# Performance work log

Hardware: AMD Instinct MI355X
Metric: run time of the kernel (lower is better)

The kernel has to match this reference:

```python
import jax, jax.numpy as jnp
import numpy as np

DIM = 192
HEADS = 4
EPS = 1e-12  # F.normalize default eps


def setup_inputs() -> dict:
    key = jax.random.key(0)
    ks = jax.random.split(key, 5)
    b, c, h, w = 8, DIM, 128, 128
    x = jax.random.normal(ks[0], (b, c, h, w), dtype=jnp.float32)
    w_qkv = jax.random.normal(ks[1], (3 * DIM, DIM, 1, 1), dtype=jnp.float32) * (1.0 / np.sqrt(DIM))
    w_dw = jax.random.normal(ks[2], (3 * DIM, 1, 3, 3), dtype=jnp.float32) * (1.0 / 3.0)
    w_proj = jax.random.normal(ks[3], (DIM, DIM, 1, 1), dtype=jnp.float32) * (1.0 / np.sqrt(DIM))
    temperature = jnp.ones((HEADS, 1, 1), dtype=jnp.float32)
    return {"x": x, "w_qkv": w_qkv, "w_dw": w_dw, "w_proj": w_proj, "temperature": temperature}


def _conv1x1(x, w):
    # x: [b,c,h,w], w: [o,c,1,1] -> [b,o,h,w]
    return jnp.einsum('bchw,oc->bohw', x, w[:, :, 0, 0])


def _dwconv3x3(x, w):
    # depthwise 3x3, padding=1; x: [b,C,h,w], w: [C,1,3,3]
    C = x.shape[1]
    return jax.lax.conv_general_dilated(
        x, w, window_strides=(1, 1), padding=((1, 1), (1, 1)),
        dimension_numbers=('NCHW', 'OIHW', 'NCHW'), feature_group_count=C)


def _l2norm(x):
    n = jnp.linalg.norm(x, axis=-1, keepdims=True)
    return x / jnp.maximum(n, EPS)


def reference(x, w_qkv, w_dw, w_proj, temperature):
    b, c, h, w = x.shape
    head = HEADS
    ch = c // head  # channels per head
    qkv = _dwconv3x3(_conv1x1(x, w_qkv), w_dw)  # [b, 3c, h, w]
    q, k, v = jnp.split(qkv, 3, axis=1)  # each [b, c, h, w]

    def to_heads(t):
        # b (head ch) h w -> b head h (ch w)
        t = t.reshape(b, head, ch, h, w)
        return t.transpose(0, 1, 3, 2, 4).reshape(b, head, h, ch * w)

    q1 = _l2norm(to_heads(q))
    k1 = _l2norm(to_heads(k))
    v1 = to_heads(v)
    # attn over height dim: [b, head, h, h]
    attn = jax.nn.softmax(jnp.einsum('bhif,bhjf->bhij', q1, k1) * temperature[None], axis=-1)
    out = jnp.einsum('bhij,bhjf->bhif', attn, v1)  # [b, head, h, ch*w]
    # b head h (ch w) -> b (head ch) h w
    out = out.reshape(b, head, h, ch, w).transpose(0, 1, 3, 2, 4).reshape(b, c, h, w)
    return _conv1x1(out, w_proj)
```

## Files before the change

### kernel.cpp

```cpp
#include <hip/hip_runtime.h>
#include <hip/hip_bf16.h>

#define BB 8
#define CC 192
#define C3 576
#define NH 4
#define CH 48
#define HH 128
#define WW 128
#define HW 16384
#define FF 6144

typedef short s16x8 __attribute__((ext_vector_type(8)));
typedef float f32x4 __attribute__((ext_vector_type(4)));

constexpr size_t SPM = 32ull * 128 * 128;

constexpr size_t OFF_XT  = 0;
constexpr size_t SZ_XT   = (size_t)BB * HW * CC * 2;
constexpr size_t OFF_WQ  = OFF_XT + SZ_XT;
constexpr size_t SZ_WQ   = (size_t)C3 * CC * 2;
constexpr size_t OFF_WP  = OFF_WQ + SZ_WQ;
constexpr size_t SZ_WP   = (size_t)CC * CC * 2;
constexpr size_t OFF_RAW = OFF_WP + SZ_WP;
constexpr size_t SZ_RAW  = (size_t)BB * C3 * HW * 2;
constexpr size_t OFF_DW  = OFF_RAW + SZ_RAW;
constexpr size_t OFF_SP  = OFF_DW + SZ_RAW;
constexpr size_t OFF_ATB = OFF_SP + 8 * SPM * 4;
constexpr size_t OFF_RQ  = OFF_ATB + 32ull * 128 * 128 * 2;
constexpr size_t OFF_RK  = OFF_RQ + 32 * 128 * 4;
constexpr size_t OFF_PS  = OFF_SP;

__device__ __forceinline__ short bf16bits(float v) {
  __hip_bfloat16 t = __float2bfloat16(v);
  return *reinterpret_cast<short*>(&t);
}
__device__ __forceinline__ float b2f(short u) {
  union { unsigned int i; float f; } x;
  x.i = ((unsigned int)(unsigned short)u) << 16;
  return x.f;
}

__device__ __forceinline__ void gload16(const void* g, void* l) {
  __builtin_amdgcn_global_load_lds((const __attribute__((address_space(1))) unsigned int*)g,
                                   (__attribute__((address_space(3))) unsigned int*)l, 16, 0, 0);
}

#define VMWAIT(N) asm volatile("s_waitcnt vmcnt(" #N ")" ::: "memory")
__device__ __forceinline__ void vmdrain() { asm volatile("s_waitcnt vmcnt(0)" ::: "memory"); }

__global__ __launch_bounds__(256) void k_cvt_t(const float* __restrict__ in,
                                               __hip_bfloat16* __restrict__ outT) {
  const int p0 = blockIdx.x * 64;
  const int c0 = blockIdx.y * 32;
  const int b = blockIdx.z;
  __shared__ float t[32][65];
  const float* ib = in + (size_t)b * CC * HW;
  const int tid = threadIdx.x;
  {
    const int c = tid >> 3, pl = (tid & 7) * 8;
    const float* s = ib + (size_t)(c0 + c) * HW + p0 + pl;
#pragma unroll
    for (int j = 0; j < 8; ++j) t[c][pl + j] = s[j];
  }
  __syncthreads();
  {
    const int pl = tid >> 2, cl = (tid & 3) * 8;
    __hip_bfloat16* d = outT + (size_t)b * HW * CC + (size_t)(p0 + pl) * CC + c0 + cl;
#pragma unroll
    for (int j = 0; j < 8; ++j) d[j] = __float2bfloat16(t[cl + j][pl]);
  }
}

__global__ __launch_bounds__(256) void k_cvt_w2(const float* __restrict__ in1, int n1,
                                                const float* __restrict__ in2, int n2,
                                                __hip_bfloat16* __restrict__ out) {
  const int i = blockIdx.x * 256 + threadIdx.x;
  if (i < n1) out[i] = __float2bfloat16(in1[i]);
  else if (i < n1 + n2) out[i] = __float2bfloat16(in2[i - n1]);
}

__global__ __launch_bounds__(256) void k_gemm(const __hip_bfloat16* __restrict__ xT,
                                              const __hip_bfloat16* __restrict__ Wb,
                                              __hip_bfloat16* __restrict__ out) {
  const int pBase = blockIdx.x * 128;
  const int mBase = blockIdx.y * 96;
  const int b = blockIdx.z;
  __shared__ char smem[43008];
  const int tid = threadIdx.x;
  const int wave = tid >> 6, lane = tid & 63;
  const int wm = wave >> 1, wn = wave & 1;
  const __hip_bfloat16* xb = xT + (size_t)b * HW * CC;
  f32x4 acc[3][4] = {};

  auto stage = [&](int k0, int buf) {
    char* Alc = smem + buf * 14336;
    char* Blc = Alc + 6144;
    {
      const int ci = tid;
      const int row = ci & 15, kg = (ci >> 4) & 3, mf = ci >> 6;
      gload16(Wb + (size_t)(mBase + mf * 16 + row) * CC + k0 + kg * 8, Alc + wave * 1024);
    }
    if (tid < 128) {
      const int ci = 256 + tid;
      const int row = ci & 15, kg = (ci >> 4) & 3, mf = ci >> 6;
      gload16(Wb + (size_t)(mBase + mf * 16 + row) * CC + k0 + kg * 8, Alc + 4096 + wave * 1024);
    }
#pragma unroll
    for (int is = 0; is < 2; ++is) {
      const int ci = is * 256 + tid;
      const int col = ci & 15, kg = (ci >> 4) & 3, nf = ci >> 6;
      gload16(xb + (size_t)(pBase + nf * 16 + col) * CC + k0 + kg * 8,
              Blc + is * 4096 + wave * 1024);
    }
  };

  stage(0, 0);
  stage(32, 1);
#pragma unroll
  for (int kc = 0; kc < 6; ++kc) {
    const int cur = kc % 3;
    if (kc < 4) stage((kc + 2) * 32, (kc + 2) % 3);
    if (kc < 4) { if (wave < 2) VMWAIT(8); else VMWAIT(6); }
    else if (kc == 4) { if (wave < 2) VMWAIT(4); else VMWAIT(3); }
    else VMWAIT(0);
    __builtin_amdgcn_s_barrier();
    char* Alc = smem + cur * 14336;
    char* Blc = Alc + 6144;
    s16x8 a[3], bf[4];
#pragma unroll
    for (int i = 0; i < 3; ++i) a[i] = *(const s16x8*)(Alc + ((wm * 3 + i) << 10) + (lane << 4));
#pragma unroll
    for (int j = 0; j < 4; ++j) bf[j] = *(const s16x8*)(Blc + ((wn * 4 + j) << 10) + (lane << 4));
#pragma unroll
    for (int i = 0; i < 3; ++i)
#pragma unroll
      for (int j = 0; j < 4; ++j)
        acc[i][j] = __builtin_amdgcn_mfma_f32_16x16x32_bf16(a[i], bf[j], acc[i][j], 0, 0, 0);
    __builtin_amdgcn_s_barrier();
  }
  short* E = (short*)smem;
  const int r0 = (lane >> 4) * 4, cl = lane & 15;
#pragma unroll
  for (int i = 0; i < 3; ++i) {
    const int lr = wm * 48 + i * 16 + r0;
#pragma unroll
    for (int j = 0; j < 4; ++j) {
      const int col = (wn * 4 + j) * 16 + cl;
#pragma unroll
      for (int r = 0; r < 4; ++r) E[(lr + r) * 136 + col] = bf16bits(acc[i][j][r]);
    }
  }
  __syncthreads();
  __hip_bfloat16* ob = out + (size_t)b * C3 * HW + pBase;
#pragma unroll
  for (int it = 0; it < 6; ++it) {
    const int vi = it * 256 + tid;
    const int row = vi >> 4, c8 = (vi & 15) * 8;
    const s16x8 v = *(const s16x8*)(E + row * 136 + c8);
    *(s16x8*)(ob + (size_t)(mBase + row) * HW + c8) = v;
  }
}

__global__ __launch_bounds__(256) void k_dwconv(const __hip_bfloat16* __restrict__ in,
                                                const float* __restrict__ wdw,
                                                __hip_bfloat16* __restrict__ out,
                                                __hip_bfloat16* __restrict__ vt,
                                                float* __restrict__ psum) {
  const int h0 = blockIdx.x * 32;
  const int c = blockIdx.y;
  const int b = blockIdx.z;
  __shared__ __hip_bfloat16 IN[34][152];
  __shared__ char TR[8192];
  const int tid = threadIdx.x;
  const __hip_bfloat16* src = in + ((size_t)b * C3 + c) * HW;
  if (tid < 68) {
    const int r = tid >> 1, col = (tid & 1) ? 136 : 0;
    *(s16x8*)(&IN[r][col]) = (s16x8){};
  }
#pragma unroll
  for (int it = 0; it < 3; ++it) {
    const int vi = it * 256 + tid;
    if (vi < 544) {
      const int r = vi >> 4, w8 = vi & 15;
      const int hg = h0 - 1 + r;
      s16x8 v = {};
      if (hg >= 0 && hg < HH) v = *(const s16x8*)(src + (size_t)hg * WW + w8 * 8);
      *(s16x8*)(&IN[r][8 + w8 * 8]) = v;
    }
  }
  const float* wp = wdw + c * 9;
  float wgt[9];
#pragma unroll
  for (int q = 0; q < 9; ++q) wgt[q] = wp[q];
  __syncthreads();

  const int hl = tid >> 3, w0 = (tid & 7) * 16;
  float res[16] = {};
#pragma unroll
  for (int dh = 0; dh < 3; ++dh) {
    const __hip_bfloat16* rp = &IN[hl + dh][0];
    const s16x8 v0 = *(const s16x8*)(rp + w0);
    const s16x8 v1 = *(const s16x8*)(rp + w0 + 8);
    const s16x8 v2 = *(const s16x8*)(rp + w0 + 16);
    const s16x8 v3 = *(const s16x8*)(rp + w0 + 24);
    float rv[18];
    rv[0] = b2f(v0[7]);
#pragma unroll
    for (int e = 0; e < 8; ++e) rv[1 + e] = b2f(v1[e]);
#pragma unroll
    for (int e = 0; e < 8; ++e) rv[9 + e] = b2f(v2[e]);
    rv[17] = b2f(v3[0]);
    const float wa = wgt[dh * 3], wb = wgt[dh * 3 + 1], wc = wgt[dh * 3 + 2];
#pragma unroll
    for (int ww = 0; ww < 16; ++ww)
      res[ww] += rv[ww] * wa + rv[ww + 1] * wb + rv[ww + 2] * wc;
  }
  if (c < 2 * CC) {
    short pk[16];
#pragma unroll
    for (int ww = 0; ww < 16; ++ww) pk[ww] = bf16bits(res[ww]);
    __hip_bfloat16* dst = out + ((size_t)b * C3 + c) * HW + (size_t)(h0 + hl) * WW + w0;
    *(s16x8*)dst = *(const s16x8*)pk;
    *(s16x8*)(dst + 8) = *(const s16x8*)(pk + 8);
    float ss = 0.f;
#pragma unroll
    for (int ww = 0; ww < 16; ++ww) ss += res[ww] * res[ww];
#pragma unroll
    for (int off = 4; off > 0; off >>= 1) ss += __shfl_down(ss, off);
    if ((tid & 7) == 0) psum[((size_t)b * HH + h0 + hl) * 384 + c] = ss;
  } else {
    const int rel = c - 2 * CC;
    const int hd = rel / CH, ch = rel - hd * CH;
#pragma unroll
    for (int ww = 0; ww < 16; ++ww) {
      const int w = w0 + ww;
      const int blk = ((w << 2) + (hl >> 3)) ^ ((w >> 3) & 3);
      *(short*)(TR + (blk << 4) + ((hl & 7) << 1)) = bf16bits(res[ww]);
    }
    __syncthreads();
    const int w = tid >> 1, hf = tid & 1;
    short ot[16];
#pragma unroll
    for (int j = 0; j < 2; ++j) {
      const int hh = hf * 16 + j * 8;
      const int blk = ((w << 2) + (hh >> 3)) ^ ((w >> 3) & 3);
      *(s16x8*)(ot + j * 8) = *(const s16x8*)(TR + (blk << 4));
    }
    __hip_bfloat16* vd = vt + ((size_t)(b * NH + hd) * FF + (size_t)ch * WW + w) * HH + h0 + hf * 16;
    *(s16x8*)vd = *(const s16x8*)ot;
    *(s16x8*)(vd + 8) = *(const s16x8*)(ot + 8);
  }
}

__global__ __launch_bounds__(64) void k_norms2(const float* __restrict__ psum,
                                               float* __restrict__ rq, float* __restrict__ rk) {
  const int i = blockIdx.x;
  const int hd = blockIdx.y;
  const int b = blockIdx.z & 7;
  const int which = blockIdx.z >> 3;
  const int lane = threadIdx.x;
  float s = 0.f;
  if (lane < 48) s = psum[((size_t)b * HH + i) * 384 + which * CC + hd * CH + lane];
#pragma unroll
  for (int off = 32; off > 0; off >>= 1) s += __shfl_down(s, off);
  if (lane == 0) {
    const float n = sqrtf(s);
    float* dst = which ? rk : rq;
    dst[(b * NH + hd) * HH + i] = 1.f / fmaxf(n, 1e-12f);
  }
}

__global__ __launch_bounds__(256) void k_qkm(const __hip_bfloat16* __restrict__ dw,
                                             float* __restrict__ sp) {
  const int ks = blockIdx.x;
  const int bh = blockIdx.y;
  const int b = bh >> 2, hd = bh & 3;
  const __hip_bfloat16* qb = dw + ((size_t)b * C3 + hd * CH) * HW;
  const __hip_bfloat16* kb = dw + ((size_t)b * C3 + CC + hd * CH) * HW;
  __shared__ char smem[49152];
  const int tid = threadIdx.x, wave = tid >> 6, lane = tid & 63;
  const int wm = wave >> 1, wn = wave & 1;
  f32x4 acc[4][4] = {};

  auto stage = [&](int chunk, int buf) {
    const int ch = ks * 6 + (chunk >> 2);
    const int w0 = (chunk & 3) * 32;
    char* Alc = smem + buf * 16384;
    char* Blc = Alc + 8192;
#pragma unroll
    for (int is = 0; is < 2; ++is) {
      const int ci = is * 256 + tid;
      const int row = ci & 15, kg = (ci >> 4) & 3, mf = ci >> 6;
      gload16(qb + (size_t)ch * HW + (mf * 16 + row) * WW + w0 + kg * 8,
              Alc + is * 4096 + wave * 1024);
    }
#pragma unroll
    for (int is = 0; is < 2; ++is) {
      const int ci = is * 256 + tid;
      const int col = ci & 15, kg = (ci >> 4) & 3, nf = ci >> 6;
      gload16(kb + (size_t)ch * HW + (nf * 16 + col) * WW + w0 + kg * 8,
              Blc + is * 4096 + wave * 1024);
    }
  };

  stage(0, 0);
  stage(1, 1);
  for (int chunk = 0; chunk < 24; ++chunk) {
    if (chunk < 22) stage(chunk + 2, (chunk + 2) % 3);
    if (chunk < 22) VMWAIT(8);
    else if (chunk == 22) VMWAIT(4);
    else VMWAIT(0);
    __builtin_amdgcn_s_barrier();
    char* Alc = smem + (chunk % 3) * 16384;
    char* Blc = Alc + 8192;
    s16x8 a[4], bf[4];
#pragma unroll
    for (int i = 0; i < 4; ++i) a[i] = *(const s16x8*)(Alc + ((wm * 4 + i) << 10) + (lane << 4));
#pragma unroll
    for (int j = 0; j < 4; ++j) bf[j] = *(const s16x8*)(Blc + ((wn * 4 + j) << 10) + (lane << 4));
#pragma unroll
    for (int i = 0; i < 4; ++i)
#pragma unroll
      for (int j = 0; j < 4; ++j)
        acc[i][j] = __builtin_amdgcn_mfma_f32_16x16x32_bf16(a[i], bf[j], acc[i][j], 0, 0, 0);
    __builtin_amdgcn_s_barrier();
  }
  float* o = sp + (size_t)ks * SPM + (size_t)bh * HH * HH;
  const int r0 = (lane >> 4) * 4, cl = lane & 15;
#pragma unroll
  for (int i = 0; i < 4; ++i)
#pragma unroll
    for (int j = 0; j < 4; ++j) {
      const int ii = wm * 64 + i * 16 + r0;
      const int jj = wn * 64 + j * 16 + cl;
#pragma unroll
      for (int r = 0; r < 4; ++r) o[(ii + r) * HH + jj] = acc[i][j][r];
    }
}

__global__ __launch_bounds__(256) void k_softmax(const float* __restrict__ sp,
                                                 const float* __restrict__ rq,
                                                 const float* __restrict__ rk,
                                                 const float* __restrict__ temp,
                                                 __hip_bfloat16* __restrict__ atb) {
  const int wave = threadIdx.x >> 6, lane = threadIdx.x & 63;
  const int i = blockIdx.x * 4 + wave;
  const int bh = blockIdx.y;
  const int hd = bh & 3;
  const size_t rowoff = ((size_t)bh * HH + i) * HH;
  float s0 = 0.f, s1 = 0.f;
#pragma unroll
  for (int ks = 0; ks < 8; ++ks) {
    s0 += sp[ks * SPM + rowoff + lane];
    s1 += sp[ks * SPM + rowoff + lane + 64];
  }
  const float scale = rq[bh * HH + i] * temp[hd];
  s0 *= scale * rk[bh * HH + lane];
  s1 *= scale * rk[bh * HH + lane + 64];
  float m = fmaxf(s0, s1);
#pragma unroll
  for (int off = 32; off > 0; off >>= 1) m = fmaxf(m, __shfl_xor(m, off));
  const float e0 = expf(s0 - m), e1 = expf(s1 - m);
  float ssum = e0 + e1;
#pragma unroll
  for (int off = 32; off > 0; off >>= 1) ssum += __shfl_xor(ssum, off);
  const float inv = 1.f / ssum;
  atb[rowoff + lane] = __float2bfloat16(e0 * inv);
  atb[rowoff + lane + 64] = __float2bfloat16(e1 * inv);
}

__global__ __launch_bounds__(256) void k_pvm(const __hip_bfloat16* __restrict__ atb,
                                             const __hip_bfloat16* __restrict__ vt,
                                             __hip_bfloat16* __restrict__ pvout) {
  const int fs = blockIdx.x;
  const int bh = blockIdx.y;
  const __hip_bfloat16* ab = atb + (size_t)bh * HH * HH;
  const __hip_bfloat16* vb = vt + ((size_t)bh * FF + fs * 128) * HH;
  __shared__ char smem[49152];
  const int tid = threadIdx.x, wave = tid >> 6, lane = tid & 63;
  const int wm = wave >> 1, wn = wave & 1;
  f32x4 acc[4][4] = {};

  auto stage = [&](int kc, int buf) {
    const int kj0 = kc * 32;
    char* Alc = smem + buf * 16384;
    char* Blc = Alc + 8192;
#pragma unroll
    for (int is = 0; is < 2; ++is) {
      const int ci = is * 256 + tid;
      const int row = ci & 15, kg = (ci >> 4) & 3, mf = ci >> 6;
      gload16(ab + (size_t)(mf * 16 + row) * HH + kj0 + kg * 8,
              Alc + is * 4096 + wave * 1024);
    }
#pragma unroll
    for (int is = 0; is < 2; ++is) {
      const int ci = is * 256 + tid;
      const int col = ci & 15, kg = (ci >> 4) & 3, nf = ci >> 6;
      gload16(vb + (size_t)(nf * 16 + col) * HH + kj0 + kg * 8,
              Blc + is * 4096 + wave * 1024);
    }
  };

  stage(0, 0);
  stage(1, 1);
#pragma unroll
  for (int kc = 0; kc < 4; ++kc) {
    if (kc < 2) stage(kc + 2, (kc + 2) % 3);
    if (kc < 2) VMWAIT(8);
    else if (kc == 2) VMWAIT(4);
    else VMWAIT(0);
    __builtin_amdgcn_s_barrier();
    char* Alc = smem + (kc % 3) * 16384;
    char* Blc = Alc + 8192;
    s16x8 a[4], bf[4];
#pragma unroll
    for (int i = 0; i < 4; ++i) a[i] = *(const s16x8*)(Alc + ((wm * 4 + i) << 10) + (lane << 4));
#pragma unroll
    for (int j = 0; j < 4; ++j) bf[j] = *(const s16x8*)(Blc + ((wn * 4 + j) << 10) + (lane << 4));
#pragma unroll
    for (int i = 0; i < 4; ++i)
#pragma unroll
      for (int j = 0; j < 4; ++j)
        acc[i][j] = __builtin_amdgcn_mfma_f32_16x16x32_bf16(a[i], bf[j], acc[i][j], 0, 0, 0);
    __builtin_amdgcn_s_barrier();
  }
  __hip_bfloat16* ob = pvout + (size_t)bh * HH * FF;
  const int r0 = (lane >> 4) * 4, cl = lane & 15;
#pragma unroll
  for (int i = 0; i < 4; ++i)
#pragma unroll
    for (int j = 0; j < 4; ++j) {
      const int ii = wm * 64 + i * 16 + r0;
      const int f = fs * 128 + (wn * 4 + j) * 16 + cl;
#pragma unroll
      for (int r = 0; r < 4; ++r) ob[(size_t)(ii + r) * FF + f] = __float2bfloat16(acc[i][j][r]);
    }
}

__global__ __launch_bounds__(256) void k_proj(const __hip_bfloat16* __restrict__ pv,
                                              const __hip_bfloat16* __restrict__ Wp,
                                              float* __restrict__ out) {
  const int i = blockIdx.x;
  const int b = blockIdx.y;
  __shared__ __hip_bfloat16 Al[6144];
  __shared__ __hip_bfloat16 Braw[12288];
  __shared__ __hip_bfloat16 Bfrag[4096];
  char* Alc = (char*)Al;
  char* Brc = (char*)Braw;
  char* Bfc = (char*)Bfrag;
  const int tid = threadIdx.x, wave = tid >> 6, lane = tid & 63;
  const int wm = wave >> 1, wn = wave & 1;
  f32x4 acc[6][4] = {};
  for (int hf = 0; hf < 2; ++hf) {
    if (hf) __syncthreads();
#pragma unroll
    for (int it = 0; it < 6; ++it) {
      const int vi = it * 256 + tid;
      const int r = vi >> 4, w8 = vi & 15;
      const int hi = (r >= 48) ? 1 : 0;
      const int hd = hf * 2 + hi, ch = r - hi * 48;
      const s16x8 v = *(const s16x8*)(pv + ((size_t)(b * NH + hd) * HH + i) * FF + ch * 128 + w8 * 8);
      *(s16x8*)(Brc + r * 256 + ((w8 ^ (r & 15)) << 4)) = v;
    }
    __syncthreads();
    for (int kc = 0; kc < 3; ++kc) {
      const int c0 = hf * 96 + kc * 32;
#pragma unroll
      for (int is = 0; is < 3; ++is) {
        const int ci = is * 256 + tid;
        const int row = ci & 15, kg = (ci >> 4) & 3, mf = ci >> 6;
        gload16(Wp + (size_t)(mf * 16 + row) * CC + c0 + kg * 8,
                Alc + is * 4096 + wave * 1024);
      }
#pragma unroll
      for (int it = 0; it < 2; ++it) {
        const int vi = it * 256 + tid;
        const int col = vi & 15, kg = (vi >> 4) & 3, nf = vi >> 6;
        const int w = nf * 16 + col;
        short tmp[8];
#pragma unroll
        for (int e = 0; e < 8; ++e) {
          const int r = (kc * 4 + kg) * 8 + e;
          tmp[e] = *(const short*)(Brc + r * 256 + (((w >> 3) ^ (r & 15)) << 4) + (w & 7) * 2);
        }
        *(s16x8*)(Bfc + ((nf * 64 + kg * 16 + col) << 4)) = *(const s16x8*)tmp;
      }
      vmdrain();
      __syncthreads();
      s16x8 a[6], bf[4];
#pragma unroll
      for (int mi = 0; mi < 6; ++mi)
        a[mi] = *(const s16x8*)(Alc + ((wm * 6 + mi) << 10) + (lane << 4));
#pragma unroll
      for (int j = 0; j < 4; ++j)
        bf[j] = *(const s16x8*)(Bfc + (((wn * 4 + j) * 64 + lane) << 4));
#pragma unroll
      for (int mi = 0; mi < 6; ++mi)
#pragma unroll
        for (int j = 0; j < 4; ++j)
          acc[mi][j] = __builtin_amdgcn_mfma_f32_16x16x32_bf16(a[mi], bf[j], acc[mi][j], 0, 0, 0);
      __syncthreads();
    }
  }
  const int r0 = (lane >> 4) * 4, cl = lane & 15;
#pragma unroll
  for (int mi = 0; mi < 6; ++mi) {
    const int o = (wm * 6 + mi) * 16 + r0;
#pragma unroll
    for (int j = 0; j < 4; ++j) {
      const int w = (wn * 4 + j) * 16 + cl;
      float* dst = out + ((size_t)b * CC + o) * HW + i * 128 + w;
#pragma unroll
      for (int r = 0; r < 4; ++r) dst[(size_t)r * HW] = acc[mi][j][r];
    }
  }
}

extern "C" void kernel_launch(void* const* d_in, const int* in_sizes, int n_in,
                              void* d_out, int out_size, void* d_ws, size_t ws_size,
                              hipStream_t stream) {
  const float* x     = (const float*)d_in[0];
  const float* wqkv  = (const float*)d_in[1];
  const float* wdw   = (const float*)d_in[2];
  const float* wproj = (const float*)d_in[3];
  const float* temp  = (const float*)d_in[4];

  char* ws = (char*)d_ws;
  __hip_bfloat16* xTb    = (__hip_bfloat16*)(ws + OFF_XT);
  __hip_bfloat16* vt     = (__hip_bfloat16*)(ws + OFF_XT);
  __hip_bfloat16* Wq     = (__hip_bfloat16*)(ws + OFF_WQ);
  __hip_bfloat16* Wp     = (__hip_bfloat16*)(ws + OFF_WP);
  __hip_bfloat16* qkvraw = (__hip_bfloat16*)(ws + OFF_RAW);
  __hip_bfloat16* pvout  = (__hip_bfloat16*)(ws + OFF_RAW);
  __hip_bfloat16* qkvdw  = (__hip_bfloat16*)(ws + OFF_DW);
  float* sp    = (float*)(ws + OFF_SP);
  float* psum  = (float*)(ws + OFF_PS);
  __hip_bfloat16* atb = (__hip_bfloat16*)(ws + OFF_ATB);
  float* rq    = (float*)(ws + OFF_RQ);
  float* rk    = (float*)(ws + OFF_RK);

  k_cvt_w2<<<dim3((C3 * CC + CC * CC + 255) / 256), 256, 0, stream>>>(wqkv, C3 * CC, wproj, CC * CC, Wq);
  k_cvt_t<<<dim3(HW / 64, CC / 32, BB), 256, 0, stream>>>(x, xTb);
  k_gemm<<<dim3(HW / 128, C3 / 96, BB), 256, 0, stream>>>(xTb, Wq, qkvraw);
  k_dwconv<<<dim3(HH / 32, C3, BB), 256, 0, stream>>>(qkvraw, wdw, qkvdw, vt, psum);
  k_norms2<<<dim3(HH, NH, 2 * BB), 64, 0, stream>>>(psum, rq, rk);
  k_qkm<<<dim3(8, 32), 256, 0, stream>>>(qkvdw, sp);
  k_softmax<<<dim3(HH / 4, 32), 256, 0, stream>>>(sp, rq, rk, temp, atb);
  k_pvm<<<dim3(48, 32), 256, 0, stream>>>(atb, vt, pvout);
  k_proj<<<dim3(HH, BB), 256, 0, stream>>>(pvout, Wp, (float*)d_out);
}
```

Baseline: 261.7 us.

## Keep A operand resident in LDS and loop over multiple output tiles

In k_gemm the full 96x192 weight tile is loaded into LDS once, and each block now processes four pixel tiles in sequence, so only the activation operand is streamed through a triple buffer. k_pvm does the same with the 128x128 attention matrix, with each block covering two feature slices. The aim is to cut redundant weight and attention reloads and per-block launch overhead. The cost is larger LDS footprint and fewer blocks (lower occupancy and parallelism), plus extra barriers around the epilogue reuse of LDS.

```diff
diff --git a/kernel.cpp b/kernel.cpp
--- a/kernel.cpp
+++ b/kernel.cpp
@@ -48,6 +48,10 @@
 
 #define VMWAIT(N) asm volatile("s_waitcnt vmcnt(" #N ")" ::: "memory")
 __device__ __forceinline__ void vmdrain() { asm volatile("s_waitcnt vmcnt(0)" ::: "memory"); }
+__device__ __forceinline__ void ldsbar() {
+  asm volatile("s_waitcnt lgkmcnt(0)" ::: "memory");
+  __builtin_amdgcn_s_barrier();
+}
 
 __global__ __launch_bounds__(256) void k_cvt_t(const float* __restrict__ in,
                                                __hip_bfloat16* __restrict__ outT) {
@@ -83,82 +87,84 @@
 __global__ __launch_bounds__(256) void k_gemm(const __hip_bfloat16* __restrict__ xT,
                                               const __hip_bfloat16* __restrict__ Wb,
                                               __hip_bfloat16* __restrict__ out) {
-  const int pBase = blockIdx.x * 128;
+  const int pG = blockIdx.x * 4;
   const int mBase = blockIdx.y * 96;
   const int b = blockIdx.z;
-  __shared__ char smem[43008];
-  const int tid = threadIdx.x;
-  const int wave = tid >> 6, lane = tid & 63;
+  __shared__ char smem[62976];
+  const int tid = threadIdx.x, wave = tid >> 6, lane = tid & 63;
   const int wm = wave >> 1, wn = wave & 1;
   const __hip_bfloat16* xb = xT + (size_t)b * HW * CC;
-  f32x4 acc[3][4] = {};
-
-  auto stage = [&](int k0, int buf) {
-    char* Alc = smem + buf * 14336;
-    char* Blc = Alc + 6144;
-    {
-      const int ci = tid;
-      const int row = ci & 15, kg = (ci >> 4) & 3, mf = ci >> 6;
-      gload16(Wb + (size_t)(mBase + mf * 16 + row) * CC + k0 + kg * 8, Alc + wave * 1024);
-    }
-    if (tid < 128) {
-      const int ci = 256 + tid;
-      const int row = ci & 15, kg = (ci >> 4) & 3, mf = ci >> 6;
-      gload16(Wb + (size_t)(mBase + mf * 16 + row) * CC + k0 + kg * 8, Alc + 4096 + wave * 1024);
-    }
+  char* Bbase = smem + 36864;
+
+#pragma unroll
+  for (int it = 0; it < 9; ++it) {
+    const int s = it * 256 + tid;
+    const int kc = s / 384, ci = s % 384;
+    const int row = ci & 15, kg = (ci >> 4) & 3, mf = ci >> 6;
+    gload16(Wb + (size_t)(mBase + mf * 16 + row) * CC + kc * 32 + kg * 8,
+            smem + it * 4096 + wave * 1024);
+  }
+
+  auto stageB = [&](int pt, int kc, int buf) {
+    char* Blc = Bbase + buf * 8192;
+    const int pBase = (pG + pt) * 128;
 #pragma unroll
     for (int is = 0; is < 2; ++is) {
       const int ci = is * 256 + tid;
       const int col = ci & 15, kg = (ci >> 4) & 3, nf = ci >> 6;
-      gload16(xb + (size_t)(pBase + nf * 16 + col) * CC + k0 + kg * 8,
+      gload16(xb + (size_t)(pBase + nf * 16 + col) * CC + kc * 32 + kg * 8,
               Blc + is * 4096 + wave * 1024);
     }
   };
 
-  stage(0, 0);
-  stage(32, 1);
-#pragma unroll
-  for (int kc = 0; kc < 6; ++kc) {
-    const int cur = kc % 3;
-    if (kc < 4) stage((kc + 2) * 32, (kc + 2) % 3);
-    if (kc < 4) { if (wave < 2) VMWAIT(8); else VMWAIT(6); }
-    else if (kc == 4) { if (wave < 2) VMWAIT(4); else VMWAIT(3); }
-    else VMWAIT(0);
-    __builtin_amdgcn_s_barrier();
-    char* Alc = smem + cur * 14336;
-    char* Blc = Alc + 6144;
-    s16x8 a[3], bf[4];
-#pragma unroll
-    for (int i = 0; i < 3; ++i) a[i] = *(const s16x8*)(Alc + ((wm * 3 + i) << 10) + (lane << 4));
-#pragma unroll
-    for (int j = 0; j < 4; ++j) bf[j] = *(const s16x8*)(Blc + ((wn * 4 + j) << 10) + (lane << 4));
-#pragma unroll
-    for (int i = 0; i < 3; ++i)
-#pragma unroll
-      for (int j = 0; j < 4; ++j)
-        acc[i][j] = __builtin_amdgcn_mfma_f32_16x16x32_bf16(a[i], bf[j], acc[i][j], 0, 0, 0);
-    __builtin_amdgcn_s_barrier();
-  }
-  short* E = (short*)smem;
+  short* E = (short*)Bbase;
   const int r0 = (lane >> 4) * 4, cl = lane & 15;
-#pragma unroll
-  for (int i = 0; i < 3; ++i) {
-    const int lr = wm * 48 + i * 16 + r0;
-#pragma unroll
-    for (int j = 0; j < 4; ++j) {
-      const int col = (wn * 4 + j) * 16 + cl;
-#pragma unroll
-      for (int r = 0; r < 4; ++r) E[(lr + r) * 136 + col] = bf16bits(acc[i][j][r]);
-    }
-  }
-  __syncthreads();
-  __hip_bfloat16* ob = out + (size_t)b * C3 * HW + pBase;
-#pragma unroll
-  for (int it = 0; it < 6; ++it) {
-    const int vi = it * 256 + tid;
-    const int row = vi >> 4, c8 = (vi & 15) * 8;
-    const s16x8 v = *(const s16x8*)(E + row * 136 + c8);
-    *(s16x8*)(ob + (size_t)(mBase + row) * HW + c8) = v;
+
+  for (int pt = 0; pt < 4; ++pt) {
+    stageB(pt, 0, 0);
+    stageB(pt, 1, 1);
+    f32x4 acc[3][4] = {};
+#pragma unroll
+    for (int kc = 0; kc < 6; ++kc) {
+      if (kc < 4) stageB(pt, kc + 2, (kc + 2) % 3);
+      if (kc < 4) VMWAIT(4);
+      else if (kc == 4) VMWAIT(2);
+      else VMWAIT(0);
+      __builtin_amdgcn_s_barrier();
+      char* Alc = smem + kc * 6144;
+      char* Blc = Bbase + (kc % 3) * 8192;
+      s16x8 a[3], bf[4];
+#pragma unroll
+      for (int i = 0; i < 3; ++i) a[i] = *(const s16x8*)(Alc + ((wm * 3 + i) << 10) + (lane << 4));
+#pragma unroll
+      for (int j = 0; j < 4; ++j) bf[j] = *(const s16x8*)(Blc + ((wn * 4 + j) << 10) + (lane << 4));
+#pragma unroll
+      for (int i = 0; i < 3; ++i)
+#pragma unroll
+        for (int j = 0; j < 4; ++j)
+          acc[i][j] = __builtin_amdgcn_mfma_f32_16x16x32_bf16(a[i], bf[j], acc[i][j], 0, 0, 0);
+      __builtin_amdgcn_s_barrier();
+    }
+#pragma unroll
+    for (int i = 0; i < 3; ++i) {
+      const int lr = wm * 48 + i * 16 + r0;
+#pragma unroll
+      for (int j = 0; j < 4; ++j) {
+        const int col = (wn * 4 + j) * 16 + cl;
+#pragma unroll
+        for (int r = 0; r < 4; ++r) E[(lr + r) * 136 + col] = bf16bits(acc[i][j][r]);
+      }
+    }
+    ldsbar();
+    __hip_bfloat16* ob = out + (size_t)b * C3 * HW + (pG + pt) * 128;
+#pragma unroll
+    for (int it = 0; it < 6; ++it) {
+      const int vi = it * 256 + tid;
+      const int row = vi >> 4, c8 = (vi & 15) * 8;
+      const s16x8 v = *(const s16x8*)(E + row * 136 + c8);
+      *(s16x8*)(ob + (size_t)(mBase + row) * HW + c8) = v;
+    }
+    ldsbar();
   }
 }
 
@@ -373,26 +379,28 @@
 __global__ __launch_bounds__(256) void k_pvm(const __hip_bfloat16* __restrict__ atb,
                                              const __hip_bfloat16* __restrict__ vt,
                                              __hip_bfloat16* __restrict__ pvout) {
-  const int fs = blockIdx.x;
+  const int fs0 = blockIdx.x * 2;
   const int bh = blockIdx.y;
   const __hip_bfloat16* ab = atb + (size_t)bh * HH * HH;
-  const __hip_bfloat16* vb = vt + ((size_t)bh * FF + fs * 128) * HH;
-  __shared__ char smem[49152];
+  __shared__ char smem[57344];
   const int tid = threadIdx.x, wave = tid >> 6, lane = tid & 63;
   const int wm = wave >> 1, wn = wave & 1;
-  f32x4 acc[4][4] = {};
-
-  auto stage = [&](int kc, int buf) {
-    const int kj0 = kc * 32;
-    char* Alc = smem + buf * 16384;
-    char* Blc = Alc + 8192;
-#pragma unroll
-    for (int is = 0; is < 2; ++is) {
-      const int ci = is * 256 + tid;
-      const int row = ci & 15, kg = (ci >> 4) & 3, mf = ci >> 6;
-      gload16(ab + (size_t)(mf * 16 + row) * HH + kj0 + kg * 8,
-              Alc + is * 4096 + wave * 1024);
-    }
+
+#pragma unroll
+  for (int it = 0; it < 8; ++it) {
+    const int s = it * 256 + tid;
+    const int kc = s >> 9, ci = s & 511;
+    const int row = ci & 15, kg = (ci >> 4) & 3, mf = ci >> 6;
+    gload16(ab + (size_t)(mf * 16 + row) * HH + kc * 32 + kg * 8,
+            smem + it * 4096 + wave * 1024);
+  }
+  char* Bbase = smem + 32768;
+
+  auto stageB = [&](int st, int buf) {
+    const int fs = fs0 + (st >> 2);
+    const int kj0 = (st & 3) * 32;
+    const __hip_bfloat16* vb = vt + ((size_t)bh * FF + fs * 128) * HH;
+    char* Blc = Bbase + buf * 8192;
 #pragma unroll
     for (int is = 0; is < 2; ++is) {
       const int ci = is * 256 + tid;
@@ -402,40 +410,45 @@
     }
   };
 
-  stage(0, 0);
-  stage(1, 1);
-#pragma unroll
-  for (int kc = 0; kc < 4; ++kc) {
-    if (kc < 2) stage(kc + 2, (kc + 2) % 3);
-    if (kc < 2) VMWAIT(8);
-    else if (kc == 2) VMWAIT(4);
-    else VMWAIT(0);
-    __builtin_amdgcn_s_barrier();
-    char* Alc = smem + (kc % 3) * 16384;
-    char* Blc = Alc + 8192;
-    s16x8 a[4], bf[4];
-#pragma unroll
-    for (int i = 0; i < 4; ++i) a[i] = *(const s16x8*)(Alc + ((wm * 4 + i) << 10) + (lane << 4));
-#pragma unroll
-    for (int j = 0; j < 4; ++j) bf[j] = *(const s16x8*)(Blc + ((wn * 4 + j) << 10) + (lane << 4));
+  stageB(0, 0);
+  stageB(1, 1);
+  const int r0 = (lane >> 4) * 4, cl = lane & 15;
+  for (int fr = 0; fr < 2; ++fr) {
+    f32x4 acc[4][4] = {};
+#pragma unroll
+    for (int kc = 0; kc < 4; ++kc) {
+      const int st = fr * 4 + kc;
+      if (st < 6) stageB(st + 2, (st + 2) % 3);
+      if (st < 6) VMWAIT(4);
+      else if (st == 6) VMWAIT(2);
+      else VMWAIT(0);
+      __builtin_amdgcn_s_barrier();
+      char* Alc = smem + kc * 8192;
+      char* Blc = Bbase + (st % 3) * 8192;
+      s16x8 a[4], bf[4];
+#pragma unroll
+      for (int i = 0; i < 4; ++i) a[i] = *(const s16x8*)(Alc + ((wm * 4 + i) << 10) + (lane << 4));
+#pragma unroll
+      for (int j = 0; j < 4; ++j) bf[j] = *(const s16x8*)(Blc + ((wn * 4 + j) << 10) + (lane << 4));
+#pragma unroll
+      for (int i = 0; i < 4; ++i)
+#pragma unroll
+        for (int j = 0; j < 4; ++j)
+          acc[i][j] = __builtin_amdgcn_mfma_f32_16x16x32_bf16(a[i], bf[j], acc[i][j], 0, 0, 0);
+      __builtin_amdgcn_s_barrier();
+    }
+    __hip_bfloat16* ob = pvout + (size_t)bh * HH * FF;
+    const int fs = fs0 + fr;
 #pragma unroll
     for (int i = 0; i < 4; ++i)
 #pragma unroll
-      for (int j = 0; j < 4; ++j)
-        acc[i][j] = __builtin_amdgcn_mfma_f32_16x16x32_bf16(a[i], bf[j], acc[i][j], 0, 0, 0);
-    __builtin_amdgcn_s_barrier();
-  }
-  __hip_bfloat16* ob = pvout + (size_t)bh * HH * FF;
-  const int r0 = (lane >> 4) * 4, cl = lane & 15;
-#pragma unroll
-  for (int i = 0; i < 4; ++i)
-#pragma unroll
-    for (int j = 0; j < 4; ++j) {
-      const int ii = wm * 64 + i * 16 + r0;
-      const int f = fs * 128 + (wn * 4 + j) * 16 + cl;
-#pragma unroll
-      for (int r = 0; r < 4; ++r) ob[(size_t)(ii + r) * FF + f] = __float2bfloat16(acc[i][j][r]);
-    }
+      for (int j = 0; j < 4; ++j) {
+        const int ii = wm * 64 + i * 16 + r0;
+        const int f = fs * 128 + (wn * 4 + j) * 16 + cl;
+#pragma unroll
+        for (int r = 0; r < 4; ++r) ob[(size_t)(ii + r) * FF + f] = __float2bfloat16(acc[i][j][r]);
+      }
+  }
 }
 
 __global__ __launch_bounds__(256) void k_proj(const __hip_bfloat16* __restrict__ pv,
@@ -542,11 +555,11 @@
 
   k_cvt_w2<<<dim3((C3 * CC + CC * CC + 255) / 256), 256, 0, stream>>>(wqkv, C3 * CC, wproj, CC * CC, Wq);
   k_cvt_t<<<dim3(HW / 64, CC / 32, BB), 256, 0, stream>>>(x, xTb);
-  k_gemm<<<dim3(HW / 128, C3 / 96, BB), 256, 0, stream>>>(xTb, Wq, qkvraw);
+  k_gemm<<<dim3(HW / 512, C3 / 96, BB), 256, 0, stream>>>(xTb, Wq, qkvraw);
   k_dwconv<<<dim3(HH / 32, C3, BB), 256, 0, stream>>>(qkvraw, wdw, qkvdw, vt, psum);
   k_norms2<<<dim3(HH, NH, 2 * BB), 64, 0, stream>>>(psum, rq, rk);
   k_qkm<<<dim3(8, 32), 256, 0, stream>>>(qkvdw, sp);
   k_softmax<<<dim3(HH / 4, 32), 256, 0, stream>>>(sp, rq, rk, temp, atb);
-  k_pvm<<<dim3(48, 32), 256, 0, stream>>>(atb, vt, pvout);
+  k_pvm<<<dim3(24, 32), 256, 0, stream>>>(atb, vt, pvout);
   k_proj<<<dim3(HH, BB), 256, 0, stream>>>(pvout, Wp, (float*)d_out);
 }
```

After: 253.3 us. 1.03x faster.
